# Kernel tuning notes

Measured on AMD Instinct MI355X. Metric: run time of the kernel, lower is better.

## Reference

```python
import jax, jax.numpy as jnp
import numpy as np

N_RBF = 32
R_CUT = 5.0
LAMBDA = 1.0

# real spherical harmonic constants
_C1 = float(np.sqrt(3.0 / (4.0 * np.pi)))            # l=1
_C2A = float(0.5 * np.sqrt(15.0 / np.pi))            # xy, yz, xz
_C2B = float(0.25 * np.sqrt(5.0 / np.pi))            # 3z^2-1
_C2C = float(0.25 * np.sqrt(15.0 / np.pi))           # x^2-y^2


def _sph_l1_l2(u):
    # u: (P,3) unit vectors -> (P, 3+5) real spherical harmonics for l=1,2
    x, y, z = u[:, 0], u[:, 1], u[:, 2]
    l1 = jnp.stack([_C1 * y, _C1 * z, _C1 * x], axis=-1)
    l2 = jnp.stack([
        _C2A * x * y,
        _C2A * y * z,
        _C2B * (3.0 * z * z - 1.0),
        _C2A * x * z,
        _C2C * (x * x - y * y),
    ], axis=-1)
    return jnp.concatenate([l1, l2], axis=-1)


def setup_inputs() -> dict:
    key = jax.random.key(0)
    k1, k2, k3, k4 = jax.random.split(key, 4)
    n, n_pairs = 100000, 3200000
    R = jax.random.normal(k1, (n, 3), dtype=jnp.float32)
    idx_i = jnp.sort(jax.random.randint(k2, (n_pairs,), 0, n, dtype=jnp.int32))
    idx_j = jax.random.randint(k3, (n_pairs,), 0, n, dtype=jnp.int32)
    z = jax.random.randint(k4, (n,), 0, 100, dtype=jnp.int32)
    pair_mask = jnp.ones((n_pairs,), dtype=jnp.float32)
    point_mask = jnp.ones((n,), dtype=jnp.float32)
    return {"R": R, "pair_mask": pair_mask, "point_mask": point_mask,
            "idx_i": idx_i, "idx_j": idx_j, "z": z}


def reference(R, pair_mask, point_mask, idx_i, idx_j, z):
    # gather + displacement, masked (safe_scale)
    r_ij = (R[idx_j] - R[idx_i]) * pair_mask[:, None]          # (P,3)
    # safe norm (avoid NaN grad at r==0)
    sq = jnp.sum(r_ij * r_ij, axis=-1)
    d_ij = jnp.where(sq == 0, 0.0, jnp.sqrt(jnp.where(sq == 0, 1.0, sq)))
    d_ij = d_ij * pair_mask                                    # (P,)

    # gaussian RBF on equidistant centers in [0, r_cut]
    centers = jnp.linspace(0.0, R_CUT, N_RBF, dtype=jnp.float32)
    width = R_CUT / N_RBF
    rbf_ij = jnp.exp(-0.5 * ((d_ij[:, None] - centers) / width) ** 2)
    rbf_ij = rbf_ij * pair_mask[:, None]                       # (P, n_rbf)

    # cosine cutoff
    phi_r_cut = 0.5 * (jnp.cos(jnp.pi * d_ij / R_CUT) + 1.0)
    phi_r_cut = phi_r_cut * (d_ij < R_CUT).astype(d_ij.dtype) * pair_mask

    # safe unit vector (safe_mask)
    denom = jnp.where(d_ij[:, None] == 0, 1.0, d_ij[:, None])
    unit_r_ij = jnp.where(d_ij[:, None] != 0, r_ij / denom, 0.0)
    unit_r_ij = unit_r_ij * pair_mask[:, None]

    # spherical harmonics for degrees [1,2]
    sph_ij = _sph_l1_l2(unit_r_ij) * pair_mask[:, None]        # (P, 8)

    # SPHC: cutoff-weighted scatter-sum per center atom (bincount over idx_i)
    weighted = sph_ij * phi_r_cut[:, None]                     # (P, 8)
    chi = jax.ops.segment_sum(weighted, idx_i, num_segments=R.shape[0])
    chi = chi * point_mask[:, None] / LAMBDA                   # (n, 8)

    return rbf_ij, chi
```

## Files before the change

kernel.cpp:

```cpp
#include <hip/hip_runtime.h>


#define NRBF 32
constexpr float R_CUT   = 5.0f;
constexpr float WIDTH   = R_CUT / NRBF;
constexpr float INV_W   = 1.0f / WIDTH;
constexpr float CSPACE  = R_CUT / (NRBF - 1);
constexpr float PI_F    = 3.14159265358979323846f;
constexpr float LOG2E   = 1.44269504088896340736f;
constexpr float EXP2_A  = -0.5f * LOG2E * INV_W * INV_W;
constexpr float C1  = 0.48860251190291992f;
constexpr float C2A = 1.09254843059207907f;
constexpr float C2B = 0.31539156525252005f;
constexpr float C2C = 0.54627421529603953f;

__global__ __launch_bounds__(256) void geom_pairs_kernel(
    const float* __restrict__ R,
    const float* __restrict__ pair_mask,
    const float* __restrict__ point_mask,
    const int*   __restrict__ idx_i,
    const int*   __restrict__ idx_j,
    float* __restrict__ rbf_out,
    float* __restrict__ chi_out,
    int n_pairs)
{
    const int p    = blockIdx.x * blockDim.x + threadIdx.x;
    const int lane = threadIdx.x & 63;

    int   seg = -1;
    float d = 0.0f, m = 0.0f;
    float w[8];
    #pragma unroll
    for (int c = 0; c < 8; ++c) w[c] = 0.0f;

    if (p < n_pairs) {
        const int i = idx_i[p];
        const int j = idx_j[p];
        m   = pair_mask[p];
        seg = i;

        const float rx = (R[3*j+0] - R[3*i+0]) * m;
        const float ry = (R[3*j+1] - R[3*i+1]) * m;
        const float rz = (R[3*j+2] - R[3*i+2]) * m;

        const float sq = rx*rx + ry*ry + rz*rz;
        d = sqrtf(sq) * m;

        float phi = 0.5f * (__cosf(PI_F * d * (1.0f/R_CUT)) + 1.0f);
        phi *= (d < R_CUT) ? 1.0f : 0.0f;
        phi *= m;

        const float inv_d = (d != 0.0f) ? (1.0f / d) : 0.0f;
        const float ux = rx * inv_d * m;
        const float uy = ry * inv_d * m;
        const float uz = rz * inv_d * m;

        float s[8];
        s[0] = C1  * uy;
        s[1] = C1  * uz;
        s[2] = C1  * ux;
        s[3] = C2A * ux * uy;
        s[4] = C2A * uy * uz;
        s[5] = C2B * (3.0f * uz * uz - 1.0f) * m;
        s[6] = C2A * ux * uz;
        s[7] = C2C * (ux * ux - uy * uy);

        const float scale = phi * point_mask[i];
        #pragma unroll
        for (int c = 0; c < 8; ++c) w[c] = s[c] * scale;
    }

    {
        const long long wbase = (long long)(p - lane);
        const int sub   = lane & 7;
        const int grp   = lane >> 3;
        #pragma unroll
        for (int it = 0; it < 8; ++it) {
            const int srcl = it * 8 + grp;
            const float dd = __shfl(d, srcl, 64);
            const float mm = __shfl(m, srcl, 64);
            const long long pr = wbase + srcl;
            if (pr < (long long)n_pairs) {
                float v[4];
                #pragma unroll
                for (int q = 0; q < 4; ++q) {
                    const int   k  = 4 * sub + q;
                    const float dc = dd - (float)k * CSPACE;
                    v[q] = __builtin_amdgcn_exp2f(EXP2_A * dc * dc) * mm;
                }
                float4* dst = (float4*)(rbf_out + pr * NRBF + 4 * sub);
                *dst = make_float4(v[0], v[1], v[2], v[3]);
            }
        }
    }

    #pragma unroll
    for (int off = 1; off < 64; off <<= 1) {
        const int  oseg = __shfl_down(seg, off, 64);
        const bool ok   = (lane + off < 64) && (oseg == seg);
        #pragma unroll
        for (int c = 0; c < 8; ++c) {
            const float ow = __shfl_down(w[c], off, 64);
            if (ok) w[c] += ow;
        }
    }
    const int  pseg = __shfl_up(seg, 1, 64);
    const bool head = (lane == 0) || (pseg != seg);
    if (head && seg >= 0) {
        float* dst = chi_out + (size_t)seg * 8;
        #pragma unroll
        for (int c = 0; c < 8; ++c) unsafeAtomicAdd(dst + c, w[c]);
    }
}

extern "C" void kernel_launch(void* const* d_in, const int* in_sizes, int n_in,
                              void* d_out, int out_size, void* d_ws, size_t ws_size,
                              hipStream_t stream) {
    const float* R          = (const float*)d_in[0];
    const float* pair_mask  = (const float*)d_in[1];
    const float* point_mask = (const float*)d_in[2];
    const int*   idx_i      = (const int*)d_in[3];
    const int*   idx_j      = (const int*)d_in[4];

    const int n_pairs = in_sizes[1];
    const int n       = in_sizes[2];

    float* rbf_out = (float*)d_out;
    float* chi_out = rbf_out + (size_t)n_pairs * NRBF;

    hipMemsetAsync(chi_out, 0, (size_t)n * 8 * sizeof(float), stream);

    const int block = 256;
    const int grid  = (n_pairs + block - 1) / block;
    geom_pairs_kernel<<<grid, block, 0, stream>>>(
        R, pair_mask, point_mask, idx_i, idx_j, rbf_out, chi_out, n_pairs);
}
```

Before: 490.5 us.

## Split fused pair kernel into separate RBF and chi kernels with nontemporal stores

The single fused kernel becomes two launches. An RBF kernel uses 8 threads per pair, each gathering R and computing its own 4 Gaussian values, then writing them with nontemporal vector stores. A separate chi kernel does the segmented scatter-sum. This drops the cross-lane shuffle loop and aims for better store throughput, at the cost of gathering R and the indices redundantly (8x in the RBF kernel, plus again in the chi kernel) and paying an extra launch.

```diff
diff --git a/kernel.cpp b/kernel.cpp
--- a/kernel.cpp
+++ b/kernel.cpp
@@ -14,21 +14,59 @@
 constexpr float C2B = 0.31539156525252005f;
 constexpr float C2C = 0.54627421529603953f;
 
-__global__ __launch_bounds__(256) void geom_pairs_kernel(
+typedef float f32x4 __attribute__((ext_vector_type(4)));
+
+__global__ __launch_bounds__(256) void rbf_kernel(
+    const float* __restrict__ R,
+    const float* __restrict__ pair_mask,
+    const int*   __restrict__ idx_i,
+    const int*   __restrict__ idx_j,
+    float*       __restrict__ rbf_out,
+    int n_pairs)
+{
+    const int t   = blockIdx.x * blockDim.x + threadIdx.x;
+    const int p   = t >> 3;
+    const int sub = t & 7;
+    if (p >= n_pairs) return;
+
+    const int   i = idx_i[p];
+    const int   j = idx_j[p];
+    const float m = pair_mask[p];
+
+    const float rx = (R[3*j+0] - R[3*i+0]) * m;
+    const float ry = (R[3*j+1] - R[3*i+1]) * m;
+    const float rz = (R[3*j+2] - R[3*i+2]) * m;
+    const float d  = sqrtf(rx*rx + ry*ry + rz*rz) * m;
+
+    const float d0 = d - (float)(4 * sub) * CSPACE;
+    const float a = d0;
+    const float b = d0 - CSPACE;
+    const float c = d0 - 2.0f * CSPACE;
+    const float e = d0 - 3.0f * CSPACE;
+
+    f32x4 v;
+    v.x = __builtin_amdgcn_exp2f(EXP2_A * a * a) * m;
+    v.y = __builtin_amdgcn_exp2f(EXP2_A * b * b) * m;
+    v.z = __builtin_amdgcn_exp2f(EXP2_A * c * c) * m;
+    v.w = __builtin_amdgcn_exp2f(EXP2_A * e * e) * m;
+
+    __builtin_nontemporal_store(
+        v, (f32x4*)(rbf_out + (size_t)p * NRBF + 4 * sub));
+}
+
+__global__ __launch_bounds__(256) void chi_kernel(
     const float* __restrict__ R,
     const float* __restrict__ pair_mask,
     const float* __restrict__ point_mask,
     const int*   __restrict__ idx_i,
     const int*   __restrict__ idx_j,
-    float* __restrict__ rbf_out,
-    float* __restrict__ chi_out,
+    float*       __restrict__ chi_out,
     int n_pairs)
 {
     const int p    = blockIdx.x * blockDim.x + threadIdx.x;
     const int lane = threadIdx.x & 63;
 
     int   seg = -1;
-    float d = 0.0f, m = 0.0f;
     float w[8];
     #pragma unroll
     for (int c = 0; c < 8; ++c) w[c] = 0.0f;
@@ -36,7 +74,7 @@
     if (p < n_pairs) {
         const int i = idx_i[p];
         const int j = idx_j[p];
-        m   = pair_mask[p];
+        const float m = pair_mask[p];
         seg = i;
 
         const float rx = (R[3*j+0] - R[3*i+0]) * m;
@@ -44,9 +82,9 @@
         const float rz = (R[3*j+2] - R[3*i+2]) * m;
 
         const float sq = rx*rx + ry*ry + rz*rz;
-        d = sqrtf(sq) * m;
+        const float d  = sqrtf(sq) * m;
 
-        float phi = 0.5f * (__cosf(PI_F * d * (1.0f/R_CUT)) + 1.0f);
+        float phi = 0.5f * (__cosf(PI_F * d * (1.0f / R_CUT)) + 1.0f);
         phi *= (d < R_CUT) ? 1.0f : 0.0f;
         phi *= m;
 
@@ -68,30 +106,6 @@
         const float scale = phi * point_mask[i];
         #pragma unroll
         for (int c = 0; c < 8; ++c) w[c] = s[c] * scale;
-    }
-
-    {
-        const long long wbase = (long long)(p - lane);
-        const int sub   = lane & 7;
-        const int grp   = lane >> 3;
-        #pragma unroll
-        for (int it = 0; it < 8; ++it) {
-            const int srcl = it * 8 + grp;
-            const float dd = __shfl(d, srcl, 64);
-            const float mm = __shfl(m, srcl, 64);
-            const long long pr = wbase + srcl;
-            if (pr < (long long)n_pairs) {
-                float v[4];
-                #pragma unroll
-                for (int q = 0; q < 4; ++q) {
-                    const int   k  = 4 * sub + q;
-                    const float dc = dd - (float)k * CSPACE;
-                    v[q] = __builtin_amdgcn_exp2f(EXP2_A * dc * dc) * mm;
-                }
-                float4* dst = (float4*)(rbf_out + pr * NRBF + 4 * sub);
-                *dst = make_float4(v[0], v[1], v[2], v[3]);
-            }
-        }
     }
 
     #pragma unroll
@@ -130,8 +144,17 @@
 
     hipMemsetAsync(chi_out, 0, (size_t)n * 8 * sizeof(float), stream);
 
-    const int block = 256;
-    const int grid  = (n_pairs + block - 1) / block;
-    geom_pairs_kernel<<<grid, block, 0, stream>>>(
-        R, pair_mask, point_mask, idx_i, idx_j, rbf_out, chi_out, n_pairs);
+    {
+        const int threads = 256;
+        const long long tot = (long long)n_pairs * 8;
+        const int grid = (int)((tot + threads - 1) / threads);
+        rbf_kernel<<<grid, threads, 0, stream>>>(
+            R, pair_mask, idx_i, idx_j, rbf_out, n_pairs);
+    }
+    {
+        const int threads = 256;
+        const int grid = (n_pairs + threads - 1) / threads;
+        chi_kernel<<<grid, threads, 0, stream>>>(
+            R, pair_mask, point_mask, idx_i, idx_j, chi_out, n_pairs);
+    }
 }
```

Measured after the change: 545.6 us. 11.2% more time.
